# Kernel tuning notes

Measured on AMD Instinct MI355X. Metric: run time of the kernel, lower is better.

The kernel has to match this reference:

```python
import jax, jax.numpy as jnp
import numpy as np

N_NODES = 50000
N_EDGES = 800000
D_IN = 128
D_HID = 128
N_CLS = 40


def setup_inputs() -> dict:
    key = jax.random.key(0)
    ks = jax.random.split(key, 9)
    x = jax.random.normal(ks[0], (N_NODES, D_IN), dtype=jnp.float32)
    edge_index = jax.random.randint(ks[1], (2, N_EDGES), 0, N_NODES, dtype=jnp.int64)
    def lin(k, fan_in, fan_out):
        bound = 1.0 / np.sqrt(fan_in)
        return jax.random.uniform(k, (fan_in, fan_out), jnp.float32, -bound, bound)
    params = {
        'w1_l': lin(ks[2], D_IN, D_HID), 'w1_r': lin(ks[3], D_IN, D_HID),
        'b1': jnp.zeros((D_HID,), jnp.float32),
        'w2_l': lin(ks[4], D_HID, D_HID), 'w2_r': lin(ks[5], D_HID, D_HID),
        'b2': jnp.zeros((D_HID,), jnp.float32),
        'w3_l': lin(ks[6], D_HID, N_CLS), 'w3_r': lin(ks[7], D_HID, N_CLS),
        'b3': jnp.zeros((N_CLS,), jnp.float32),
    }
    return {'x': x, 'edge_index': edge_index, **params}


def _sage_layer(x, src, dst, w_l, w_r, b):
    # mean-aggregate messages from src -> dst, then lin_l(agg) + lin_r(x) + b, relu
    msgs = x[src]                                             # [E, d] gather
    agg = jax.ops.segment_sum(msgs, dst, num_segments=x.shape[0])  # [N, d]
    deg = jax.ops.segment_sum(jnp.ones((src.shape[0],), x.dtype), dst,
                              num_segments=x.shape[0])        # [N]
    agg = agg / jnp.maximum(deg, 1.0)[:, None]
    out = agg @ w_l + x @ w_r + b
    return jax.nn.relu(out)  # dropout p=0.0 -> identity


def reference(x, edge_index, w1_l, w1_r, b1, w2_l, w2_r, b2, w3_l, w3_r, b3):
    src, dst = edge_index[0], edge_index[1]
    h = _sage_layer(x, src, dst, w1_l, w1_r, b1)
    h = _sage_layer(h, src, dst, w2_l, w2_r, b2)
    h = _sage_layer(h, src, dst, w3_l, w3_r, b3)
    return h
```

## Files before the change

kernel.cpp:

```cpp
#include <hip/hip_runtime.h>
#include <hip/hip_bf16.h>

#define NN 50000
#define NE 800000
#define DD 128
#define NCLS 40
#define NBK ((NN + 255) >> 8)
#define EPB 1024
#define PB ((NE + EPB - 1) / EPB)
#define CVB ((NN * DD / 4) / 256)
#define WB 384
#define SEMAX 5120

typedef _Float16 f16x8 __attribute__((ext_vector_type(8)));
typedef _Float16 f16x4 __attribute__((ext_vector_type(4)));
typedef float f32x4 __attribute__((ext_vector_type(4)));

__device__ __forceinline__ unsigned int pack2h(_Float16 a, _Float16 b) {
    union { _Float16 h[2]; unsigned int u; } c;
    c.h[0] = a; c.h[1] = b;
    return c.u;
}
__device__ __forceinline__ void unpack2h(unsigned int p, float& a, float& b) {
    union { unsigned int u; _Float16 h[2]; } c;
    c.u = p;
    a = (float)c.h[0]; b = (float)c.h[1];
}

__global__ void k_front(const int* __restrict__ ei, int* __restrict__ cellcnt,
                        int* __restrict__ celloff, unsigned int* __restrict__ pairs,
                        const float* __restrict__ x, unsigned short* __restrict__ xh,
                        const float* __restrict__ w1l, const float* __restrict__ w1r,
                        const float* __restrict__ w2l, const float* __restrict__ w2r,
                        const float* __restrict__ w3l, const float* __restrict__ w3r,
                        unsigned short* __restrict__ bt1h,
                        unsigned short* __restrict__ bt2h,
                        unsigned short* __restrict__ bt3h) {
    if (blockIdx.x >= PB + CVB) {
        int idx = blockIdx.x - (PB + CVB);
        int w = idx >> 1, half = idx & 1;
        int ks = w & 7, tmp = w >> 3;
        int nt = tmp & 7, layer = tmp >> 3;
        const int NT = (layer == 2) ? 3 : 8;
        const int NC = (layer == 2) ? NCLS : DD;
        if (nt >= NT) return;
        const float* wl = (layer == 0) ? w1l : (layer == 1) ? w2l : w3l;
        const float* wr = (layer == 0) ? w1r : (layer == 1) ? w2r : w3r;
        unsigned short* bh = (layer == 0) ? bt1h : (layer == 1) ? bt2h : bt3h;
        int t = threadIdx.x;
        int j = t & 7, lane = (t >> 3) + half * 32;
        int row = nt * 16 + (lane & 15);
        int k = ks * 32 + (lane >> 4) * 8 + j;
        float v = 0.f;
        if (row < NC)
            v = (k < 128) ? wl[(size_t)k * NC + row] : wr[(size_t)(k - 128) * NC + row];
        union { _Float16 f; unsigned short u; } ch;
        ch.f = (_Float16)v;
        bh[((size_t)(ks * NT + nt) * 64 + lane) * 8 + j] = ch.u;
        return;
    }
    if (blockIdx.x >= PB) {
        int i = (blockIdx.x - PB) * 256 + threadIdx.x;
        float4 v = ((const float4*)x)[i];
        f16x4 h;
        h[0] = (_Float16)v.x; h[1] = (_Float16)v.y;
        h[2] = (_Float16)v.z; h[3] = (_Float16)v.w;
        *(f16x4*)(xh + (size_t)i * 4) = h;
        return;
    }
    __shared__ int hist[NBK];
    __shared__ int s[256];
    __shared__ unsigned int sE[EPB];
    __shared__ int nz;
    const int t = threadIdx.x, blk = blockIdx.x;
    const int e0 = blk * EPB;
    if (t == 0) nz = 0;
    for (int i = t; i < NBK; i += 256) hist[i] = 0;
    __syncthreads();
    int any = 0;
    for (int i = t; i < EPB; i += 256)
        if (ei[2 * e0 + 2 * i + 1] != 0) any = 1;
    if (any) atomicOr(&nz, 1);
    __syncthreads();
    const int is64 = (nz == 0);
    unsigned int v[EPB / 256];
    int eb[EPB / 256], er[EPB / 256];
#pragma unroll
    for (int j = 0; j < EPB / 256; ++j) {
        int e = e0 + j * 256 + t;
        if (e < NE) {
            int sv, d;
            if (is64) { sv = ei[2 * e]; d = ei[2 * (NE + e)]; }
            else      { sv = ei[e];     d = ei[NE + e]; }
            v[j] = ((unsigned)sv << 16) | (unsigned)d;
            eb[j] = d >> 8;
            er[j] = atomicAdd(&hist[eb[j]], 1);
        } else {
            eb[j] = -1;
        }
    }
    __syncthreads();
    int hv = (t < NBK) ? hist[t] : 0;
    s[t] = hv;
    __syncthreads();
#pragma unroll
    for (int off = 1; off < 256; off <<= 1) {
        int u = (t >= off) ? s[t - off] : 0;
        __syncthreads();
        s[t] += u;
        __syncthreads();
    }
#pragma unroll
    for (int j = 0; j < EPB / 256; ++j)
        if (eb[j] >= 0) sE[s[eb[j]] - hist[eb[j]] + er[j]] = v[j];
    __syncthreads();
    ((uint4*)(pairs + (size_t)blk * EPB))[t] = ((const uint4*)sE)[t];
    for (int i = t; i < NBK; i += 256) {
        cellcnt[(size_t)i * PB + blk] = hist[i];
        celloff[(size_t)i * PB + blk] = s[i] - hist[i];
    }
}

__global__ void k_scan_ba(const int* __restrict__ cellcnt, int* __restrict__ bsum) {
    __shared__ int red[256];
    int b = blockIdx.x, t = threadIdx.x;
    int acc = 0;
    for (int i = t; i < PB; i += 256) acc += cellcnt[(size_t)b * PB + i];
    red[t] = acc;
    __syncthreads();
#pragma unroll
    for (int off = 128; off > 0; off >>= 1) {
        if (t < off) red[t] += red[t + off];
        __syncthreads();
    }
    if (t == 0) bsum[b] = red[0];
}

__global__ void k_fill2(const unsigned int* __restrict__ pairs,
                        const int* __restrict__ cellcnt,
                        const int* __restrict__ celloff,
                        const int* __restrict__ bsum,
                        int* __restrict__ row_ptr, unsigned short* __restrict__ srcs) {
    __shared__ unsigned int sE[SEMAX];
    __shared__ int hist[256];
    __shared__ int cur[256];
    __shared__ int sb[256];
    __shared__ int scnt;
    const int b = blockIdx.x, t = threadIdx.x;
    if (t < 256) {
        int v = (t < NBK) ? bsum[t] : 0;
        sb[t] = v;
    }
    if (t == 0) scnt = 0;
    if (t < 256) hist[t] = 0;
    __syncthreads();
#pragma unroll
    for (int off = 1; off < 256; off <<= 1) {
        int u = (t >= off && t < 256) ? sb[t - off] : 0;
        __syncthreads();
        if (t < 256) sb[t] += u;
        __syncthreads();
    }
    const int bbase = (b == 0) ? 0 : sb[b - 1];
    if (b == NBK - 1 && t == 0) row_ptr[NN] = sb[NBK - 1];
    for (int blk = t; blk < PB; blk += 512) {
        int cnt = cellcnt[(size_t)b * PB + blk];
        if (cnt) {
            int off = celloff[(size_t)b * PB + blk];
            int base = atomicAdd(&scnt, cnt);
            if (base + cnt <= SEMAX) {
                const unsigned int* pp = pairs + (size_t)blk * EPB + off;
                for (int j = 0; j < cnt; ++j) {
                    unsigned int v = pp[j];
                    sE[base + j] = v;
                    atomicAdd(&hist[v & 255u], 1);
                }
            }
        }
    }
    __syncthreads();
    int h = (t < 256) ? hist[t] : 0;
    if (t < 256) cur[t] = h;
    __syncthreads();
#pragma unroll
    for (int off = 1; off < 256; off <<= 1) {
        int u = (t >= off && t < 256) ? cur[t - off] : 0;
        __syncthreads();
        if (t < 256) cur[t] += u;
        __syncthreads();
    }
    if (t < 256) {
        int node = (b << 8) + t;
        int base = bbase + cur[t] - h;
        if (node < NN) row_ptr[node] = base;
        cur[t] = base;
    }
    __syncthreads();
    int total = min(scnt, SEMAX);
    for (int i = t; i < total; i += 512) {
        unsigned int v = sE[i];
        int pos = atomicAdd(&cur[v & 255u], 1);
        srcs[pos] = (unsigned short)(v >> 16);
    }
}

template <int J>
__device__ __forceinline__ void acc4(const uint4* __restrict__ tab,
                                     const unsigned short* __restrict__ srcs,
                                     int i, int eg, int cg, float* a) {
    uint4 p[J];
#pragma unroll
    for (int j = 0; j < J; ++j)
        p[j] = tab[(size_t)srcs[i + j * 4 + eg] * 16 + cg];
#pragma unroll
    for (int j = 0; j < J; ++j) {
        float u0, u1;
        unpack2h(p[j].x, u0, u1); a[0] += u0; a[1] += u1;
        unpack2h(p[j].y, u0, u1); a[2] += u0; a[3] += u1;
        unpack2h(p[j].z, u0, u1); a[4] += u0; a[5] += u1;
        unpack2h(p[j].w, u0, u1); a[6] += u0; a[7] += u1;
    }
}

__global__ __launch_bounds__(256, 8)
void k_agg(const unsigned int* __restrict__ inh, const int* __restrict__ row_ptr,
           const unsigned short* __restrict__ srcs, unsigned int* __restrict__ oh) {
    int node = blockIdx.x * 4 + (threadIdx.x >> 6);
    if (node >= NN) return;
    int lane = threadIdx.x & 63;
    int eg = lane >> 4, cg = lane & 15;
    const uint4* tab = (const uint4*)inh;
    int b = row_ptr[node], e = row_ptr[node + 1];
    int deg = e - b;
    float a[8] = {};
    int i = b;
    while (i + 16 <= e) { acc4<4>(tab, srcs, i, eg, cg, a); i += 16; }
    if (i + 8 <= e) { acc4<2>(tab, srcs, i, eg, cg, a); i += 8; }
    if (i + 4 <= e) { acc4<1>(tab, srcs, i, eg, cg, a); i += 4; }
    int rem = e - i;
    if (rem > 0) {
        int idx = i + eg;
        if (idx > e - 1) idx = e - 1;
        uint4 p = tab[(size_t)srcs[idx] * 16 + cg];
        if (eg < rem) {
            float u0, u1;
            unpack2h(p.x, u0, u1); a[0] += u0; a[1] += u1;
            unpack2h(p.y, u0, u1); a[2] += u0; a[3] += u1;
            unpack2h(p.z, u0, u1); a[4] += u0; a[5] += u1;
            unpack2h(p.w, u0, u1); a[6] += u0; a[7] += u1;
        }
    }
#pragma unroll
    for (int k = 0; k < 8; ++k) {
        a[k] += __shfl_xor(a[k], 16);
        a[k] += __shfl_xor(a[k], 32);
    }
    if (eg == 0) {
        float inv = 1.0f / (float)(deg > 0 ? deg : 1);
        uint4 o;
        o.x = pack2h((_Float16)(a[0] * inv), (_Float16)(a[1] * inv));
        o.y = pack2h((_Float16)(a[2] * inv), (_Float16)(a[3] * inv));
        o.z = pack2h((_Float16)(a[4] * inv), (_Float16)(a[5] * inv));
        o.w = pack2h((_Float16)(a[6] * inv), (_Float16)(a[7] * inv));
        ((uint4*)oh)[(size_t)node * 16 + cg] = o;
    }
}

template <int NT, int KPS, bool PACKOUT>
__launch_bounds__(256, 4)
__global__ void k_mfma(const unsigned short* __restrict__ A1h,
                       const unsigned short* __restrict__ A2h,
                       const unsigned short* __restrict__ Bthf,
                       const float* __restrict__ bias, float* __restrict__ outf,
                       unsigned short* __restrict__ outh, const int NC) {
    constexpr int STAGE_ELEMS = KPS * NT * 64 * 8;
    constexpr int STAGE_U4 = STAGE_ELEMS / 8;
    __shared__ unsigned short sBh[STAGE_ELEMS];

    const int tid = threadIdx.x;
    const int wave = tid >> 6, lane = tid & 63;
    const int quad = lane >> 4, mr = lane & 15;
    const int m0 = blockIdx.x * 64 + wave * 16;
    const int row = m0 + mr;
    const bool rok = row < NN;

    f32x4 acc[NT] = {};
    const f16x8 zero = {};

    auto aload = [&](int ks) -> f16x8 {
        const int ko = ((ks * 32) & 127) + quad * 8;
        const unsigned short* base = (ks < 4) ? A1h : A2h;
        return rok ? *(const f16x8*)(base + (size_t)row * 128 + ko) : zero;
    };

    f16x8 cah = aload(0), pah;

#pragma unroll
    for (int s = 0; s < 8 / KPS; ++s) {
        const uint4* gh = (const uint4*)(Bthf + (size_t)s * STAGE_ELEMS);
        uint4* lh = (uint4*)sBh;
        if (s) __syncthreads();
        for (int i = tid; i < STAGE_U4; i += 256) lh[i] = gh[i];
        __syncthreads();

#pragma unroll
        for (int kl = 0; kl < KPS; ++kl) {
            const int ks = s * KPS + kl;
            if (ks < 7) pah = aload(ks + 1);
#pragma unroll
            for (int n = 0; n < NT; ++n) {
                const int fo = ((kl * NT + n) * 64 + lane) * 8;
                f16x8 bh = *(const f16x8*)(sBh + fo);
                acc[n] = __builtin_amdgcn_mfma_f32_16x16x32_f16(cah, bh, acc[n], 0, 0, 0);
            }
            cah = pah;
        }
    }

#pragma unroll
    for (int n = 0; n < NT; ++n) {
        int col = n * 16 + mr;
        float bv = (col < NC) ? bias[col] : 0.f;
#pragma unroll
        for (int r = 0; r < 4; ++r) {
            int orow = m0 + quad * 4 + r;
            if (orow < NN && col < NC) {
                float v = acc[n][r] + bv;
                v = v > 0.f ? v : 0.f;
                if (PACKOUT) {
                    union { _Float16 f; unsigned short u; } ch;
                    ch.f = (_Float16)v;
                    outh[(size_t)orow * 128 + col] = ch.u;
                } else {
                    outf[(size_t)orow * NC + col] = v;
                }
            }
        }
    }
}

__global__ __launch_bounds__(256, 4)
void k_gemm3(const unsigned short* __restrict__ Ah,
             const unsigned short* __restrict__ Bthf,
             const float* __restrict__ bias,
             unsigned short* __restrict__ zh, float* __restrict__ yf) {
    __shared__ unsigned short sBh[8 * 3 * 64 * 8];
    const int tid = threadIdx.x;
    const int wave = tid >> 6, lane = tid & 63;
    const int quad = lane >> 4, mr = lane & 15;
    const int m0 = blockIdx.x * 64 + wave * 16;
    const int row = m0 + mr;
    const bool rok = row < NN;

    const uint4* gh = (const uint4*)Bthf;
    uint4* lh = (uint4*)sBh;
    for (int i = tid; i < (8 * 3 * 64 * 8) / 8; i += 256) lh[i] = gh[i];

    const f16x8 zero = {};
    f16x8 a[4];
#pragma unroll
    for (int j = 0; j < 4; ++j)
        a[j] = rok ? *(const f16x8*)(Ah + (size_t)row * 128 + j * 32 + quad * 8)
                   : zero;
    __syncthreads();

    f32x4 accl[3] = {}, accr[3] = {};
#pragma unroll
    for (int ks = 0; ks < 4; ++ks) {
#pragma unroll
        for (int n = 0; n < 3; ++n) {
            f16x8 bl = *(const f16x8*)(sBh + ((ks * 3 + n) * 64 + lane) * 8);
            accl[n] = __builtin_amdgcn_mfma_f32_16x16x32_f16(a[ks], bl, accl[n], 0, 0, 0);
            f16x8 br = *(const f16x8*)(sBh + (((ks + 4) * 3 + n) * 64 + lane) * 8);
            accr[n] = __builtin_amdgcn_mfma_f32_16x16x32_f16(a[ks], br, accr[n], 0, 0, 0);
        }
    }

#pragma unroll
    for (int n = 0; n < 3; ++n) {
        int col = n * 16 + mr;
        float bv = (col < NCLS) ? bias[col] : 0.f;
#pragma unroll
        for (int r = 0; r < 4; ++r) {
            int orow = m0 + quad * 4 + r;
            if (orow < NN) {
                union { _Float16 f; unsigned short u; } ch;
                ch.f = (_Float16)accl[n][r];
                zh[(size_t)orow * 64 + col] = ch.u;
                if (col < NCLS) yf[(size_t)orow * 40 + col] = accr[n][r] + bv;
            }
        }
    }
}

template <int J>
__device__ __forceinline__ void acc3(const uint2* __restrict__ tab,
                                     const unsigned short* __restrict__ srcs,
                                     int i, int eg, int cg, float* a) {
    uint2 p[J];
#pragma unroll
    for (int j = 0; j < J; ++j)
        p[j] = tab[(size_t)srcs[i + j * 4 + eg] * 16 + cg];
#pragma unroll
    for (int j = 0; j < J; ++j) {
        float u0, u1;
        unpack2h(p[j].x, u0, u1); a[0] += u0; a[1] += u1;
        unpack2h(p[j].y, u0, u1); a[2] += u0; a[3] += u1;
    }
}

__global__ __launch_bounds__(256, 8)
void k_agg3(const unsigned int* __restrict__ zu,
            const int* __restrict__ row_ptr,
            const unsigned short* __restrict__ srcs,
            const float* __restrict__ yf, float* __restrict__ out) {
    const int node = blockIdx.x * 4 + (threadIdx.x >> 6);
    const int lane = threadIdx.x & 63;
    const int eg = lane >> 4, cg = lane & 15;
    const uint2* tab = (const uint2*)zu;
    const int b = row_ptr[node], e = row_ptr[node + 1];
    const int deg = e - b;
    float a[4] = {};
    int i = b;
    while (i + 16 <= e) { acc3<4>(tab, srcs, i, eg, cg, a); i += 16; }
    if (i + 8 <= e) { acc3<2>(tab, srcs, i, eg, cg, a); i += 8; }
    if (i + 4 <= e) { acc3<1>(tab, srcs, i, eg, cg, a); i += 4; }
    int rem = e - i;
    if (rem > 0) {
        int idx = i + eg;
        if (idx > e - 1) idx = e - 1;
        uint2 p = tab[(size_t)srcs[idx] * 16 + cg];
        if (eg < rem) {
            float u0, u1;
            unpack2h(p.x, u0, u1); a[0] += u0; a[1] += u1;
            unpack2h(p.y, u0, u1); a[2] += u0; a[3] += u1;
        }
    }
#pragma unroll
    for (int k = 0; k < 4; ++k) {
        a[k] += __shfl_xor(a[k], 16);
        a[k] += __shfl_xor(a[k], 32);
    }
    if (eg == 0 && cg < 10) {
        float inv = 1.0f / (float)(deg > 0 ? deg : 1);
        float4 yv = ((const float4*)yf)[(size_t)node * 10 + cg];
        float4 o;
        o.x = fmaxf(a[0] * inv + yv.x, 0.f);
        o.y = fmaxf(a[1] * inv + yv.y, 0.f);
        o.z = fmaxf(a[2] * inv + yv.z, 0.f);
        o.w = fmaxf(a[3] * inv + yv.w, 0.f);
        ((float4*)out)[(size_t)node * 10 + cg] = o;
    }
}

extern "C" void kernel_launch(void* const* d_in, const int* in_sizes, int n_in,
                              void* d_out, int out_size, void* d_ws, size_t ws_size,
                              hipStream_t stream) {
    const float* x    = (const float*)d_in[0];
    const int*   ei   = (const int*)d_in[1];
    const float* w1_l = (const float*)d_in[2];
    const float* w1_r = (const float*)d_in[3];
    const float* b1   = (const float*)d_in[4];
    const float* w2_l = (const float*)d_in[5];
    const float* w2_r = (const float*)d_in[6];
    const float* b2   = (const float*)d_in[7];
    const float* w3_l = (const float*)d_in[8];
    const float* w3_r = (const float*)d_in[9];
    const float* b3   = (const float*)d_in[10];
    float* out = (float*)d_out;

    char* w = (char*)d_ws;
    size_t off = 0;
    auto alloc = [&](size_t bytes) -> void* {
        void* p = w + off;
        off += (bytes + 255) / 256 * 256;
        return p;
    };
    int* row_ptr = (int*)alloc((size_t)(NN + 1) * 4);
    unsigned short* srcs = (unsigned short*)alloc((size_t)NE * 2 + 64);
    int* cellcnt = (int*)alloc((size_t)NBK * PB * 4);
    int* celloff = (int*)alloc((size_t)NBK * PB * 4);
    int* bsum    = (int*)alloc((size_t)NBK * 4);
    unsigned int* pairs = (unsigned int*)alloc((size_t)PB * EPB * 4);
    unsigned short* xh   = (unsigned short*)alloc((size_t)NN * DD * 2);
    unsigned short* aggh = (unsigned short*)alloc((size_t)NN * DD * 2);
    unsigned short* h1h  = (unsigned short*)alloc((size_t)NN * DD * 2);
    unsigned short* zh   = (unsigned short*)alloc((size_t)NN * 64 * 2);
    float*          yf   = (float*)alloc((size_t)NN * 40 * 4);
    unsigned short* bt1h = (unsigned short*)alloc((size_t)8 * 8 * 64 * 8 * 2);
    unsigned short* bt2h = (unsigned short*)alloc((size_t)8 * 8 * 64 * 8 * 2);
    unsigned short* bt3h = (unsigned short*)alloc((size_t)8 * 3 * 64 * 8 * 2);
    unsigned short* h2h = xh;
    (void)ws_size;

    k_front<<<PB + CVB + WB, 256, 0, stream>>>(ei, cellcnt, celloff, pairs, x, xh,
                                               w1_l, w1_r, w2_l, w2_r, w3_l, w3_r,
                                               bt1h, bt2h, bt3h);
    k_scan_ba<<<NBK, 256, 0, stream>>>(cellcnt, bsum);
    k_fill2<<<NBK, 512, 0, stream>>>(pairs, cellcnt, celloff, bsum, row_ptr, srcs);

    const int gmb = (NN + 63) / 64;
    const int gab = (NN + 3) / 4;
    k_agg<<<gab, 256, 0, stream>>>((const unsigned int*)xh, row_ptr, srcs,
                                   (unsigned int*)aggh);
    k_mfma<8, 4, true><<<gmb, 256, 0, stream>>>(aggh, xh, bt1h, b1,
                                                nullptr, h1h, DD);
    k_agg<<<gab, 256, 0, stream>>>((const unsigned int*)h1h, row_ptr, srcs,
                                   (unsigned int*)aggh);
    k_mfma<8, 4, true><<<gmb, 256, 0, stream>>>(aggh, h1h, bt2h, b2,
                                                nullptr, h2h, DD);
    k_gemm3<<<gmb, 256, 0, stream>>>(h2h, bt3h, b3, zh, yf);
    k_agg3<<<NN / 4, 256, 0, stream>>>((const unsigned int*)zh, row_ptr, srcs,
                                       yf, out);
}
```

Measured before the change: 236.0 us.

## Split feature tables into column planes and aggregate per plane with LDS-staged sources

Feature buffers are stored as four 32-column planes of fp16, each with a zero padding row, instead of row-major 128-wide rows. A new aggregation kernel assigns blocks to (plane, 16-node chunk), stages up to 48 source indices per node in shared memory padded with the zero row, and gathers 64-byte plane slices so each plane's table stays cache-resident. This targets the cache misses of random gathers over the full 12.8 MB table. In exchange each gather is narrower (4 bytes per lane), work is padded to the max degree in each group of four nodes, and the GEMM kernels now read strided planes.

```diff
diff --git a/kernel.cpp b/kernel.cpp
--- a/kernel.cpp
+++ b/kernel.cpp
@@ -11,6 +11,8 @@
 #define CVB ((NN * DD / 4) / 256)
 #define WB 384
 #define SEMAX 5120
+#define PR (NN + 1)
+#define DCAP 48
 
 typedef _Float16 f16x8 __attribute__((ext_vector_type(8)));
 typedef _Float16 f16x4 __attribute__((ext_vector_type(4)));
@@ -26,6 +28,7 @@
     c.u = p;
     a = (float)c.h[0]; b = (float)c.h[1];
 }
+
 
 __global__ void k_front(const int* __restrict__ ei, int* __restrict__ cellcnt,
                         int* __restrict__ celloff, unsigned int* __restrict__ pairs,
@@ -35,9 +38,20 @@
                         const float* __restrict__ w3l, const float* __restrict__ w3r,
                         unsigned short* __restrict__ bt1h,
                         unsigned short* __restrict__ bt2h,
-                        unsigned short* __restrict__ bt3h) {
+                        unsigned short* __restrict__ bt3h,
+                        unsigned short* __restrict__ h1h) {
     if (blockIdx.x >= PB + CVB) {
         int idx = blockIdx.x - (PB + CVB);
+        if (idx == WB) {
+            int t = threadIdx.x;
+            if (t < 128) {
+                int which = t >> 4;
+                unsigned int* buf = (unsigned int*)((which < 4) ? xh : h1h);
+                int plane = which & 3;
+                buf[((size_t)plane * PR + NN) * 16 + (t & 15)] = 0u;
+            }
+            return;
+        }
         int w = idx >> 1, half = idx & 1;
         int ks = w & 7, tmp = w >> 3;
         int nt = tmp & 7, layer = tmp >> 3;
@@ -65,7 +79,11 @@
         f16x4 h;
         h[0] = (_Float16)v.x; h[1] = (_Float16)v.y;
         h[2] = (_Float16)v.z; h[3] = (_Float16)v.w;
-        *(f16x4*)(xh + (size_t)i * 4) = h;
+        int row = i >> 5;
+        int f = i & 31;
+        int plane = f >> 3;
+        int pc = (f & 7) * 4;
+        *(f16x4*)(xh + ((size_t)plane * PR + row) * 32 + pc) = h;
         return;
     }
     __shared__ int hist[NBK];
@@ -204,66 +222,70 @@
     }
 }
 
-template <int J>
-__device__ __forceinline__ void acc4(const uint4* __restrict__ tab,
-                                     const unsigned short* __restrict__ srcs,
-                                     int i, int eg, int cg, float* a) {
-    uint4 p[J];
-#pragma unroll
-    for (int j = 0; j < J; ++j)
-        p[j] = tab[(size_t)srcs[i + j * 4 + eg] * 16 + cg];
-#pragma unroll
-    for (int j = 0; j < J; ++j) {
+__global__ __launch_bounds__(256, 8)
+void k_aggp(const unsigned int* __restrict__ inq, const int* __restrict__ row_ptr,
+            const unsigned short* __restrict__ srcs, unsigned int* __restrict__ oq) {
+    __shared__ unsigned short sSrc[16 * DCAP];
+    __shared__ int sRp[17];
+    const int t = threadIdx.x;
+    const int plane = (blockIdx.x & 7) >> 1;
+    const int c = ((blockIdx.x >> 3) << 1) + (blockIdx.x & 1);
+    if (c >= NN / 16) return;
+    const int n0 = c * 16;
+    if (t < 17) sRp[t] = row_ptr[n0 + t];
+    __syncthreads();
+    {
+        int ln = t >> 4, k2 = t & 15;
+        int b = sRp[ln], e = sRp[ln + 1];
+#pragma unroll
+        for (int m = 0; m < DCAP / 16; ++m) {
+            int k = k2 + m * 16;
+            sSrc[ln * DCAP + k] = (b + k < e) ? srcs[b + k] : (unsigned short)NN;
+        }
+    }
+    __syncthreads();
+    const int wave = t >> 6, lane = t & 63;
+    const int ng = lane >> 4;
+    const unsigned int pc = lane & 15;
+    const int ln = (wave << 2) + ng;
+    const unsigned int* __restrict__ tab = inq + (size_t)plane * (PR * 16);
+    const int b = sRp[ln], e = sRp[ln + 1];
+    const int deg = e - b;
+    int dm = deg;
+    dm = max(dm, __shfl_xor(dm, 16));
+    dm = max(dm, __shfl_xor(dm, 32));
+    const int capped = min(dm, DCAP);
+    const int nit = (capped + 3) >> 2;
+    float a0 = 0.f, a1 = 0.f;
+    int sb = ln * DCAP;
+    for (int it = 0; it < nit; ++it) {
+        unsigned int s0 = sSrc[sb + 0];
+        unsigned int s1 = sSrc[sb + 1];
+        unsigned int s2 = sSrc[sb + 2];
+        unsigned int s3 = sSrc[sb + 3];
+        unsigned int p0 = tab[s0 * 16u + pc];
+        unsigned int p1 = tab[s1 * 16u + pc];
+        unsigned int p2 = tab[s2 * 16u + pc];
+        unsigned int p3 = tab[s3 * 16u + pc];
         float u0, u1;
-        unpack2h(p[j].x, u0, u1); a[0] += u0; a[1] += u1;
-        unpack2h(p[j].y, u0, u1); a[2] += u0; a[3] += u1;
-        unpack2h(p[j].z, u0, u1); a[4] += u0; a[5] += u1;
-        unpack2h(p[j].w, u0, u1); a[6] += u0; a[7] += u1;
-    }
-}
-
-__global__ __launch_bounds__(256, 8)
-void k_agg(const unsigned int* __restrict__ inh, const int* __restrict__ row_ptr,
-           const unsigned short* __restrict__ srcs, unsigned int* __restrict__ oh) {
-    int node = blockIdx.x * 4 + (threadIdx.x >> 6);
-    if (node >= NN) return;
-    int lane = threadIdx.x & 63;
-    int eg = lane >> 4, cg = lane & 15;
-    const uint4* tab = (const uint4*)inh;
-    int b = row_ptr[node], e = row_ptr[node + 1];
-    int deg = e - b;
-    float a[8] = {};
-    int i = b;
-    while (i + 16 <= e) { acc4<4>(tab, srcs, i, eg, cg, a); i += 16; }
-    if (i + 8 <= e) { acc4<2>(tab, srcs, i, eg, cg, a); i += 8; }
-    if (i + 4 <= e) { acc4<1>(tab, srcs, i, eg, cg, a); i += 4; }
-    int rem = e - i;
-    if (rem > 0) {
-        int idx = i + eg;
-        if (idx > e - 1) idx = e - 1;
-        uint4 p = tab[(size_t)srcs[idx] * 16 + cg];
-        if (eg < rem) {
+        unpack2h(p0, u0, u1); a0 += u0; a1 += u1;
+        unpack2h(p1, u0, u1); a0 += u0; a1 += u1;
+        unpack2h(p2, u0, u1); a0 += u0; a1 += u1;
+        unpack2h(p3, u0, u1); a0 += u0; a1 += u1;
+        sb += 4;
+    }
+    if (dm > DCAP) {
+        for (int k = DCAP; k < deg; ++k) {
+            unsigned int s = (unsigned int)srcs[b + k];
+            unsigned int p = tab[s * 16u + pc];
             float u0, u1;
-            unpack2h(p.x, u0, u1); a[0] += u0; a[1] += u1;
-            unpack2h(p.y, u0, u1); a[2] += u0; a[3] += u1;
-            unpack2h(p.z, u0, u1); a[4] += u0; a[5] += u1;
-            unpack2h(p.w, u0, u1); a[6] += u0; a[7] += u1;
-        }
-    }
-#pragma unroll
-    for (int k = 0; k < 8; ++k) {
-        a[k] += __shfl_xor(a[k], 16);
-        a[k] += __shfl_xor(a[k], 32);
-    }
-    if (eg == 0) {
-        float inv = 1.0f / (float)(deg > 0 ? deg : 1);
-        uint4 o;
-        o.x = pack2h((_Float16)(a[0] * inv), (_Float16)(a[1] * inv));
-        o.y = pack2h((_Float16)(a[2] * inv), (_Float16)(a[3] * inv));
-        o.z = pack2h((_Float16)(a[4] * inv), (_Float16)(a[5] * inv));
-        o.w = pack2h((_Float16)(a[6] * inv), (_Float16)(a[7] * inv));
-        ((uint4*)oh)[(size_t)node * 16 + cg] = o;
-    }
+            unpack2h(p, u0, u1);
+            a0 += u0; a1 += u1;
+        }
+    }
+    float inv = 1.0f / (float)(deg > 0 ? deg : 1);
+    unsigned int ov = pack2h((_Float16)(a0 * inv), (_Float16)(a1 * inv));
+    __builtin_nontemporal_store(ov, &oq[((size_t)plane * PR + (n0 + ln)) * 16 + pc]);
 }
 
 template <int NT, int KPS, bool PACKOUT>
@@ -288,9 +310,10 @@
     const f16x8 zero = {};
 
     auto aload = [&](int ks) -> f16x8 {
-        const int ko = ((ks * 32) & 127) + quad * 8;
         const unsigned short* base = (ks < 4) ? A1h : A2h;
-        return rok ? *(const f16x8*)(base + (size_t)row * 128 + ko) : zero;
+        const int plane = ks & 3;
+        return rok ? *(const f16x8*)(base + ((size_t)plane * PR + row) * 32 + quad * 8)
+                   : zero;
     };
 
     f16x8 cah = aload(0), pah;
@@ -330,7 +353,8 @@
                 if (PACKOUT) {
                     union { _Float16 f; unsigned short u; } ch;
                     ch.f = (_Float16)v;
-                    outh[(size_t)orow * 128 + col] = ch.u;
+                    int pl = col >> 5, pcc = col & 31;
+                    outh[((size_t)pl * PR + orow) * 32 + pcc] = ch.u;
                 } else {
                     outf[(size_t)orow * NC + col] = v;
                 }
@@ -360,7 +384,7 @@
     f16x8 a[4];
 #pragma unroll
     for (int j = 0; j < 4; ++j)
-        a[j] = rok ? *(const f16x8*)(Ah + (size_t)row * 128 + j * 32 + quad * 8)
+        a[j] = rok ? *(const f16x8*)(Ah + ((size_t)j * PR + row) * 32 + quad * 8)
                    : zero;
     __syncthreads();
 
@@ -482,9 +506,9 @@
     int* celloff = (int*)alloc((size_t)NBK * PB * 4);
     int* bsum    = (int*)alloc((size_t)NBK * 4);
     unsigned int* pairs = (unsigned int*)alloc((size_t)PB * EPB * 4);
-    unsigned short* xh   = (unsigned short*)alloc((size_t)NN * DD * 2);
-    unsigned short* aggh = (unsigned short*)alloc((size_t)NN * DD * 2);
-    unsigned short* h1h  = (unsigned short*)alloc((size_t)NN * DD * 2);
+    unsigned short* xh   = (unsigned short*)alloc((size_t)4 * PR * 32 * 2);
+    unsigned short* aggh = (unsigned short*)alloc((size_t)4 * PR * 32 * 2);
+    unsigned short* h1h  = (unsigned short*)alloc((size_t)4 * PR * 32 * 2);
     unsigned short* zh   = (unsigned short*)alloc((size_t)NN * 64 * 2);
     float*          yf   = (float*)alloc((size_t)NN * 40 * 4);
     unsigned short* bt1h = (unsigned short*)alloc((size_t)8 * 8 * 64 * 8 * 2);
@@ -493,19 +517,19 @@
     unsigned short* h2h = xh;
     (void)ws_size;
 
-    k_front<<<PB + CVB + WB, 256, 0, stream>>>(ei, cellcnt, celloff, pairs, x, xh,
-                                               w1_l, w1_r, w2_l, w2_r, w3_l, w3_r,
-                                               bt1h, bt2h, bt3h);
+    k_front<<<PB + CVB + WB + 1, 256, 0, stream>>>(ei, cellcnt, celloff, pairs, x, xh,
+                                                   w1_l, w1_r, w2_l, w2_r, w3_l, w3_r,
+                                                   bt1h, bt2h, bt3h, h1h);
     k_scan_ba<<<NBK, 256, 0, stream>>>(cellcnt, bsum);
     k_fill2<<<NBK, 512, 0, stream>>>(pairs, cellcnt, celloff, bsum, row_ptr, srcs);
 
     const int gmb = (NN + 63) / 64;
-    const int gab = (NN + 3) / 4;
-    k_agg<<<gab, 256, 0, stream>>>((const unsigned int*)xh, row_ptr, srcs,
+    const int gp  = 8 * ((NN / 16 + 1) / 2);
+    k_aggp<<<gp, 256, 0, stream>>>((const unsigned int*)xh, row_ptr, srcs,
                                    (unsigned int*)aggh);
     k_mfma<8, 4, true><<<gmb, 256, 0, stream>>>(aggh, xh, bt1h, b1,
                                                 nullptr, h1h, DD);
-    k_agg<<<gab, 256, 0, stream>>>((const unsigned int*)h1h, row_ptr, srcs,
+    k_aggp<<<gp, 256, 0, stream>>>((const unsigned int*)h1h, row_ptr, srcs,
                                    (unsigned int*)aggh);
     k_mfma<8, 4, true><<<gmb, 256, 0, stream>>>(aggh, h1h, bt2h, b2,
                                                 nullptr, h2h, DD);
```

Result: faster. 227.3 us (-3.7%).
